# Kernel tuning notes

Hardware: AMD Instinct MI355X
Metric: run time of the kernel (lower is better)

Reference implementation:

```python
import jax, jax.numpy as jnp
import numpy as np

NU = 200000   # num user nodes
NI = 200000   # num item nodes
E = 500000    # edges per relation
D = 128       # in_feats
H = 128       # h_feats
NEG_SLOPE = 0.01  # F.leaky_relu default


def _sage(x_src, x_dst, src, dst, n_dst, W_self, W_neigh, b):
    # DGL SAGEConv('mean'): fc_self(x_dst) + fc_neigh(mean of in-neighbors) + bias
    msg = x_src[src]                                   # [E, d] gather
    agg = jax.ops.segment_sum(msg, dst, num_segments=n_dst)   # [n_dst, d]
    deg = jax.ops.segment_sum(jnp.ones((src.shape[0],), x_src.dtype), dst,
                              num_segments=n_dst)      # [n_dst]
    mean = agg / jnp.maximum(deg, 1.0)[:, None]        # zero in-degree -> 0
    return x_dst @ W_self + mean @ W_neigh + b


def setup_inputs() -> dict:
    key = jax.random.key(0)
    ks = jax.random.split(key, 20)
    s = 1.0 / np.sqrt(D)
    inp = {
        'x_user': jax.random.normal(ks[0], (NU, D), jnp.float32),
        'x_item': jax.random.normal(ks[1], (NI, D), jnp.float32),
        'w1_self_uc': jax.random.normal(ks[2], (D, H), jnp.float32) * s,
        'w1_neigh_uc': jax.random.normal(ks[3], (D, H), jnp.float32) * s,
        'b1_uc': jnp.zeros((H,), jnp.float32),
        'w1_self_iu': jax.random.normal(ks[4], (D, H), jnp.float32) * s,
        'w1_neigh_iu': jax.random.normal(ks[5], (D, H), jnp.float32) * s,
        'b1_iu': jnp.zeros((H,), jnp.float32),
        'w2_self_uc': jax.random.normal(ks[6], (H, H), jnp.float32) * s,
        'w2_neigh_uc': jax.random.normal(ks[7], (H, H), jnp.float32) * s,
        'b2_uc': jnp.zeros((H,), jnp.float32),
        'w2_self_iu': jax.random.normal(ks[8], (H, H), jnp.float32) * s,
        'w2_neigh_iu': jax.random.normal(ks[9], (H, H), jnp.float32) * s,
        'b2_iu': jnp.zeros((H,), jnp.float32),
        'src_uc': jax.random.randint(ks[10], (E,), 0, NU, jnp.int32),
        'dst_uc': jax.random.randint(ks[11], (E,), 0, NI, jnp.int32),
        'src_iu': jax.random.randint(ks[12], (E,), 0, NI, jnp.int32),
        'dst_iu': jax.random.randint(ks[13], (E,), 0, NU, jnp.int32),
    }
    return inp


def reference(x_user, x_item,
              w1_self_uc, w1_neigh_uc, b1_uc, w1_self_iu, w1_neigh_iu, b1_iu,
              w2_self_uc, w2_neigh_uc, b2_uc, w2_self_iu, w2_neigh_iu, b2_iu,
              src_uc, dst_uc, src_iu, dst_iu):
    # layer 1: relation 'clicks' user->item, relation 'clicked_by' item->user
    h1_item = _sage(x_user, x_item, src_uc, dst_uc, NI, w1_self_uc, w1_neigh_uc, b1_uc)
    h1_user = _sage(x_item, x_user, src_iu, dst_iu, NU, w1_self_iu, w1_neigh_iu, b1_iu)
    h1_item = jax.nn.leaky_relu(h1_item, NEG_SLOPE)
    h1_user = jax.nn.leaky_relu(h1_user, NEG_SLOPE)
    # layer 2
    h2_item = _sage(h1_user, h1_item, src_uc, dst_uc, NI, w2_self_uc, w2_neigh_uc, b2_uc)
    h2_user = _sage(h1_item, h1_user, src_iu, dst_iu, NU, w2_self_iu, w2_neigh_iu, b2_iu)
    # stack [user, item] (same shape) for a single output tensor
    return jnp.stack([h2_user, h2_item], axis=0)  # [2, 200000, 128]
```

## Files before the change

kernel.cpp:

```cpp
#include <hip/hip_runtime.h>
#include <hip/hip_bf16.h>

#define D_ 128

typedef __attribute__((ext_vector_type(8))) short s8b;
typedef __attribute__((ext_vector_type(4))) float f4;

union U4 { uint u[4]; s8b v; uint4 q; };

__device__ __forceinline__ void gl16(const void* g, void* lds) {
    __builtin_amdgcn_global_load_lds(
        (const __attribute__((address_space(1))) void*)g,
        (__attribute__((address_space(3))) void*)lds, 16, 0, 0);
}

__device__ __forceinline__ void split2(float f0, float f1, uint& hp, uint& lp) {
    uint u0 = __float_as_uint(f0), u1 = __float_as_uint(f1);
    hp = (u0 >> 16) | (u1 & 0xffff0000u);
    float r0 = f0 - __uint_as_float(u0 & 0xffff0000u);
    float r1 = f1 - __uint_as_float(u1 & 0xffff0000u);
    uint v0 = __float_as_uint(r0), v1 = __float_as_uint(r1);
    uint l0 = (v0 + 0x7fffu + ((v0 >> 16) & 1u)) >> 16;
    uint l1 = (v1 + 0x7fffu + ((v1 >> 16) & 1u)) >> 16;
    lp = l0 | (l1 << 16);
}

__device__ __forceinline__ float4 asf4(uint4 u) {
    return make_float4(__uint_as_float(u.x), __uint_as_float(u.y),
                       __uint_as_float(u.z), __uint_as_float(u.w));
}

__global__ void deg2_kernel(const int* __restrict__ dstA, const int* __restrict__ dstB,
                            int* __restrict__ degA, int* __restrict__ degB, int E) {
    int e = blockIdx.x * blockDim.x + threadIdx.x;
    const int* dst = blockIdx.y ? dstB : dstA;
    int* deg = blockIdx.y ? degB : degA;
    if (e < E) atomicAdd(&deg[dst[e]], 1);
}

__global__ __launch_bounds__(256)
void scan1m(const int* __restrict__ degA, const int* __restrict__ degB,
            int* __restrict__ rpA, int* __restrict__ rpB,
            int* __restrict__ partA, int* __restrict__ partB, int N) {
    const int* deg = blockIdx.y ? degB : degA;
    int* rp = blockIdx.y ? rpB : rpA;
    int* partials = blockIdx.y ? partB : partA;
    int tid = threadIdx.x;
    int i = blockIdx.x * 256 + tid;
    int v = (i < N) ? deg[i] : 0;
    int lane = tid & 63, wid = tid >> 6;
    int x = v;
#pragma unroll
    for (int off = 1; off < 64; off <<= 1) {
        int y = __shfl_up(x, off, 64);
        if (lane >= off) x += y;
    }
    __shared__ int wsum[5];
    if (lane == 63) wsum[wid] = x;
    __syncthreads();
    if (tid == 0) {
        int a = wsum[0], b = wsum[1], c = wsum[2], d = wsum[3];
        wsum[0] = 0; wsum[1] = a; wsum[2] = a + b; wsum[3] = a + b + c;
        wsum[4] = a + b + c + d;
    }
    __syncthreads();
    if (i < N) rp[i] = wsum[wid] + x - v;
    if (tid == 0) partials[blockIdx.x] = wsum[4];
}

__global__ __launch_bounds__(1024)
void scan2m(int* __restrict__ partA, int* __restrict__ partB, int B) {
    int* partials = blockIdx.x ? partB : partA;
    __shared__ int buf[1024];
    int t = threadIdx.x;
    int v = (t < B) ? partials[t] : 0;
    buf[t] = v;
    __syncthreads();
    for (int off = 1; off < 1024; off <<= 1) {
        int add = (t >= off) ? buf[t - off] : 0;
        __syncthreads();
        buf[t] += add;
        __syncthreads();
    }
    if (t < B) partials[t] = buf[t] - v;
}

__global__ __launch_bounds__(256)
void scan3m(int* __restrict__ rpA, int* __restrict__ rpB,
            const int* __restrict__ partA, const int* __restrict__ partB, int N, int E) {
    int* rp = blockIdx.y ? rpB : rpA;
    const int* partials = blockIdx.y ? partB : partA;
    int i = blockIdx.x * 256 + threadIdx.x;
    if (i < N) rp[i] += partials[blockIdx.x];
    if (i == 0) rp[N] = E;
}

__global__ void fill2_csr(const int* __restrict__ srcA, const int* __restrict__ dstA,
                          const int* __restrict__ rpA, int* __restrict__ curA,
                          int* __restrict__ colA, int* __restrict__ colpA,
                          const int* __restrict__ srcB, const int* __restrict__ dstB,
                          const int* __restrict__ rpB, int* __restrict__ curB,
                          int* __restrict__ colB, int* __restrict__ colpB, int E) {
    int e = blockIdx.x * blockDim.x + threadIdx.x;
    if (e >= E) return;
    const int* src = blockIdx.y ? srcB : srcA;
    const int* dst = blockIdx.y ? dstB : dstA;
    const int* rp  = blockIdx.y ? rpB : rpA;
    int* cursor = blockIdx.y ? curB : curA;
    int* col    = blockIdx.y ? colB : colA;
    int* colp   = blockIdx.y ? colpB : colpA;
    int d = dst[e];
    int s = src[e];
    int idx = atomicAdd(&cursor[d], 1);
    col[rp[d] + idx] = s;
    if (idx < 4) colp[d * 4 + idx] = s;
}

__global__ __launch_bounds__(256)
void prep_weights(const float* __restrict__ s0, const float* __restrict__ n0,
                  const float* __restrict__ s1, const float* __restrict__ n1,
                  const float* __restrict__ s2, const float* __restrict__ n2,
                  const float* __restrict__ s3, const float* __restrict__ n3,
                  ushort* __restrict__ WTH, ushort* __restrict__ WTL) {
    int g = blockIdx.y;
    int t = blockIdx.x * 256 + threadIdx.x;
    int c = t & 127;
    int oct = t >> 7;
    const float* self  = g == 0 ? s0 : g == 1 ? s1 : g == 2 ? s2 : s3;
    const float* neigh = g == 0 ? n0 : g == 1 ? n1 : g == 2 ? n2 : n3;
    uint hd[4], ld_[4];
#pragma unroll
    for (int p = 0; p < 4; ++p) {
        uint hpair = 0, lpair = 0;
#pragma unroll
        for (int q = 0; q < 2; ++q) {
            int kv = oct * 8 + p * 2 + q;
            const float* Wsrc = kv < 128 ? self : neigh;
            float f = Wsrc[(size_t)(kv & 127) * 128 + c];
            uint u = __float_as_uint(f);
            uint h = u >> 16;
            float r = f - __uint_as_float(u & 0xffff0000u);
            uint v = __float_as_uint(r);
            uint l = (v + 0x7fffu + ((v >> 16) & 1u)) >> 16;
            hpair |= h << (16 * q);
            lpair |= l << (16 * q);
        }
        hd[p] = hpair; ld_[p] = lpair;
    }
    size_t base = ((size_t)g * 128 + c) * 256 + oct * 8;
    *(uint4*)(WTH + base) = make_uint4(hd[0], hd[1], hd[2], hd[3]);
    *(uint4*)(WTL + base) = make_uint4(ld_[0], ld_[1], ld_[2], ld_[3]);
}

#define AGGH 0
#define AGGL 16384
#define ASTEP 32768
#define WHO 40960
#define WLO 49152

template<int FP32IN, int SPLIT, int LRELU>
__device__ __forceinline__ void fused_body(const char* A1, const char* XN,
        const int* rp, const int* col, const int* colp,
        const ushort* WTh, const ushort* WTl, const float* bias, void* outp,
        int bid, char* smem) {
    const int t = threadIdx.x;
    const int row0 = bid * 64;
    const int li = t & 15;

    uint4 GH[2][4], GL[2][4];
    float wv[2][4];
    int begv[2], endv[2], dgv[2];
#pragma unroll
    for (int p = 0; p < 2; ++p) {
        int nl = p * 32 + (t >> 4);
        int node = row0 + nl;
        int beg = rp[node], end = rp[node + 1];
        int dg = end - beg;
        begv[p] = beg; endv[p] = end; dgv[p] = dg;
        int4 c4 = *(const int4*)(colp + (size_t)node * 4);
        int s0 = dg > 0 ? c4.x : 0;
        int s1 = dg > 1 ? c4.y : 0;
        int s2 = dg > 2 ? c4.z : 0;
        int s3 = dg > 3 ? c4.w : 0;
        wv[p][0] = dg > 0 ? 1.f : 0.f;
        wv[p][1] = dg > 1 ? 1.f : 0.f;
        wv[p][2] = dg > 2 ? 1.f : 0.f;
        wv[p][3] = dg > 3 ? 1.f : 0.f;
        const int lo = FP32IN ? li * 32 : li * 16;
        const int d2 = FP32IN ? 16 : 256;
        const char* p0 = XN + (size_t)s0 * 512 + lo;
        const char* p1 = XN + (size_t)s1 * 512 + lo;
        const char* p2 = XN + (size_t)s2 * 512 + lo;
        const char* p3 = XN + (size_t)s3 * 512 + lo;
        GH[p][0] = *(const uint4*)p0; GL[p][0] = *(const uint4*)(p0 + d2);
        GH[p][1] = *(const uint4*)p1; GL[p][1] = *(const uint4*)(p1 + d2);
        GH[p][2] = *(const uint4*)p2; GL[p][2] = *(const uint4*)(p2 + d2);
        GH[p][3] = *(const uint4*)p3; GL[p][3] = *(const uint4*)(p3 + d2);
    }

    auto stage = [&](int ks) {
        if (ks < 4) {
            if (FP32IN) {
                int row = t >> 3, cs = t & 7;
                gl16(A1 + (size_t)(row0 + row) * 512 + ks * 128 + ((cs ^ (row & 7)) * 16),
                     smem + ASTEP + t * 16);
            } else {
                int j = t & 255, part = t >> 8;
                int row = j >> 2, cs = j & 3;
                gl16(A1 + (size_t)(row0 + row) * 512 + part * 256 + ks * 64
                         + ((cs ^ ((row >> 1) & 3)) * 16),
                     smem + ASTEP + part * 4096 + j * 16);
            }
        }
        {
            int col_ = t >> 2, cs = t & 3;
            size_t so = (size_t)col_ * 512 + ks * 64 + ((cs ^ ((col_ >> 1) & 3)) * 16);
            gl16((const char*)WTh + so, smem + WHO + t * 16);
            gl16((const char*)WTl + so, smem + WLO + t * 16);
        }
    };

    const int w = t >> 6, lane = t & 63;
    const int fr = lane & 15, hi = lane >> 4;
    const int mrow0 = (w & 1) * 32, ncol0 = (w >> 1) * 32;

    f4 acc[2][2];
    {
        float bv[2];
#pragma unroll
        for (int n = 0; n < 2; ++n) bv[n] = bias[ncol0 + n * 16 + fr];
#pragma unroll
        for (int m = 0; m < 2; ++m)
#pragma unroll
            for (int n = 0; n < 2; ++n) acc[m][n] = (f4){bv[n], bv[n], bv[n], bv[n]};
    }

    auto compute = [&](int ks) {
        s8b ah[2], al[2], wh[2], wl[2];
        if (ks < 4) {
            if (FP32IN) {
#pragma unroll
                for (int m = 0; m < 2; ++m) {
                    int r = mrow0 + m * 16 + fr;
                    f4 x0 = *(const f4*)(smem + ASTEP + r * 128 + (((hi * 2) ^ (r & 7)) * 16));
                    f4 x1 = *(const f4*)(smem + ASTEP + r * 128 + (((hi * 2 + 1) ^ (r & 7)) * 16));
                    U4 H, L;
                    split2(x0[0], x0[1], H.u[0], L.u[0]);
                    split2(x0[2], x0[3], H.u[1], L.u[1]);
                    split2(x1[0], x1[1], H.u[2], L.u[2]);
                    split2(x1[2], x1[3], H.u[3], L.u[3]);
                    ah[m] = H.v; al[m] = L.v;
                }
            } else {
#pragma unroll
                for (int m = 0; m < 2; ++m) {
                    int r = mrow0 + m * 16 + fr;
                    int off = r * 64 + ((hi ^ ((r >> 1) & 3)) * 16);
                    ah[m] = *(const s8b*)(smem + ASTEP + off);
                    al[m] = *(const s8b*)(smem + ASTEP + 4096 + off);
                }
            }
        } else {
            int kk = ks - 4;
#pragma unroll
            for (int m = 0; m < 2; ++m) {
                int r = mrow0 + m * 16 + fr;
                int chunk = (kk * 4 + hi) ^ (r & 3) ^ (((r >> 2) & 3) << 2);
                ah[m] = *(const s8b*)(smem + AGGH + r * 256 + chunk * 16);
                al[m] = *(const s8b*)(smem + AGGL + r * 256 + chunk * 16);
            }
        }
#pragma unroll
        for (int n = 0; n < 2; ++n) {
            int c = ncol0 + n * 16 + fr;
            int off = c * 64 + ((hi ^ ((c >> 1) & 3)) * 16);
            wh[n] = *(const s8b*)(smem + WHO + off);
            wl[n] = *(const s8b*)(smem + WLO + off);
        }
#pragma unroll
        for (int n = 0; n < 2; ++n)
#pragma unroll
            for (int m = 0; m < 2; ++m) {
                acc[m][n] = __builtin_amdgcn_mfma_f32_16x16x32_bf16(ah[m], wh[n], acc[m][n], 0, 0, 0);
                acc[m][n] = __builtin_amdgcn_mfma_f32_16x16x32_bf16(al[m], wh[n], acc[m][n], 0, 0, 0);
                acc[m][n] = __builtin_amdgcn_mfma_f32_16x16x32_bf16(ah[m], wl[n], acc[m][n], 0, 0, 0);
            }
    };

    stage(0);
    __syncthreads();

#pragma unroll
    for (int p = 0; p < 2; ++p) {
        int nl = p * 32 + (t >> 4);
        float a[8];
#pragma unroll
        for (int j = 0; j < 8; ++j) a[j] = 0.f;
        if (FP32IN) {
#pragma unroll
            for (int q = 0; q < 4; ++q) {
                float4 X = asf4(GH[p][q]);
                float4 Y = asf4(GL[p][q]);
                float wq = wv[p][q];
                a[0] = fmaf(X.x, wq, a[0]); a[1] = fmaf(X.y, wq, a[1]);
                a[2] = fmaf(X.z, wq, a[2]); a[3] = fmaf(X.w, wq, a[3]);
                a[4] = fmaf(Y.x, wq, a[4]); a[5] = fmaf(Y.y, wq, a[5]);
                a[6] = fmaf(Y.z, wq, a[6]); a[7] = fmaf(Y.w, wq, a[7]);
            }
            for (int e = begv[p] + 4; e < endv[p]; ++e) {
                const char* pp = XN + (size_t)col[e] * 512 + li * 32;
                float4 X = *(const float4*)pp, Y = *(const float4*)(pp + 16);
                a[0] += X.x; a[1] += X.y; a[2] += X.z; a[3] += X.w;
                a[4] += Y.x; a[5] += Y.y; a[6] += Y.z; a[7] += Y.w;
            }
        } else {
#pragma unroll
            for (int q = 0; q < 4; ++q) {
                float wq = wv[p][q];
                const ushort* hu = (const ushort*)&GH[p][q];
                const ushort* lu = (const ushort*)&GL[p][q];
#pragma unroll
                for (int j = 0; j < 8; ++j) {
                    float v = __uint_as_float((uint)hu[j] << 16)
                            + __uint_as_float((uint)lu[j] << 16);
                    a[j] = fmaf(v, wq, a[j]);
                }
            }
            for (int e = begv[p] + 4; e < endv[p]; ++e) {
                const char* pp = XN + (size_t)col[e] * 512 + li * 16;
                uint4 H = *(const uint4*)pp, L = *(const uint4*)(pp + 256);
                const ushort* hu = (const ushort*)&H;
                const ushort* lu = (const ushort*)&L;
#pragma unroll
                for (int j = 0; j < 8; ++j)
                    a[j] += __uint_as_float((uint)hu[j] << 16)
                          + __uint_as_float((uint)lu[j] << 16);
            }
        }
        float inv = 1.f / (float)(dgv[p] > 0 ? dgv[p] : 1);
        uint h[4], l[4];
        split2(a[0] * inv, a[1] * inv, h[0], l[0]);
        split2(a[2] * inv, a[3] * inv, h[1], l[1]);
        split2(a[4] * inv, a[5] * inv, h[2], l[2]);
        split2(a[6] * inv, a[7] * inv, h[3], l[3]);
        int chunk = li ^ (nl & 3) ^ (((nl >> 2) & 3) << 2);
        *(uint4*)(smem + AGGH + nl * 256 + chunk * 16) = make_uint4(h[0], h[1], h[2], h[3]);
        *(uint4*)(smem + AGGL + nl * 256 + chunk * 16) = make_uint4(l[0], l[1], l[2], l[3]);
    }

    compute(0);
    __syncthreads();
    for (int ks = 1; ks < 8; ++ks) {
        stage(ks);
        __syncthreads();
        compute(ks);
        __syncthreads();
    }

    float* T = (float*)smem;
#pragma unroll
    for (int m = 0; m < 2; ++m)
#pragma unroll
        for (int n = 0; n < 2; ++n)
#pragma unroll
            for (int r = 0; r < 4; ++r)
                T[(mrow0 + m * 16 + hi * 4 + r) * 132 + ncol0 + n * 16 + fr] = acc[m][n][r];
    __syncthreads();
    {
        int row = t >> 3, q = t & 7;
        int gr = row0 + row;
        if (SPLIT) {
            char* ob = (char*)outp + (size_t)gr * 512;
#pragma unroll
            for (int i = 0; i < 2; ++i) {
                const float* p = T + row * 132 + (q * 2 + i) * 8;
                f4 x0 = *(const f4*)p;
                f4 x1 = *(const f4*)(p + 4);
                float e[8] = {x0[0], x0[1], x0[2], x0[3], x1[0], x1[1], x1[2], x1[3]};
                if (LRELU) {
#pragma unroll
                    for (int j = 0; j < 8; ++j) e[j] = e[j] > 0.f ? e[j] : 0.01f * e[j];
                }
                uint h[4], l[4];
#pragma unroll
                for (int j = 0; j < 4; ++j) split2(e[2 * j], e[2 * j + 1], h[j], l[j]);
                *(uint4*)(ob + (q * 2 + i) * 16) = make_uint4(h[0], h[1], h[2], h[3]);
                *(uint4*)(ob + 256 + (q * 2 + i) * 16) = make_uint4(l[0], l[1], l[2], l[3]);
            }
        } else {
            float* ob = (float*)outp + (size_t)gr * 128;
#pragma unroll
            for (int i = 0; i < 4; ++i) {
                f4 x = *(const f4*)(T + row * 132 + q * 16 + i * 4);
                float e0 = x[0], e1 = x[1], e2 = x[2], e3 = x[3];
                if (LRELU) {
                    e0 = e0 > 0.f ? e0 : 0.01f * e0;
                    e1 = e1 > 0.f ? e1 : 0.01f * e1;
                    e2 = e2 > 0.f ? e2 : 0.01f * e2;
                    e3 = e3 > 0.f ? e3 : 0.01f * e3;
                }
                *(float4*)(ob + q * 16 + i * 4) = make_float4(e0, e1, e2, e3);
            }
        }
    }
}

template<int FP32IN, int SPLIT, int LRELU>
__global__ __launch_bounds__(512, 4)
void fused2k(const void* A1a, const void* XNa, const int* rpA, const int* colA,
             const int* colpA, const ushort* WTha, const ushort* WTla,
             const float* ba, void* outa,
             const void* A1b, const void* XNb, const int* rpB, const int* colB,
             const int* colpB, const ushort* WThb, const ushort* WTlb,
             const float* bb, void* outb, int blocksA) {
    __shared__ __align__(16) char smem[57344];
    bool isA = (int)blockIdx.x < blocksA;
    int bid = isA ? blockIdx.x : blockIdx.x - blocksA;
    if (isA)
        fused_body<FP32IN, SPLIT, LRELU>((const char*)A1a, (const char*)XNa, rpA, colA,
                                         colpA, WTha, WTla, ba, outa, bid, smem);
    else
        fused_body<FP32IN, SPLIT, LRELU>((const char*)A1b, (const char*)XNb, rpB, colB,
                                         colpB, WThb, WTlb, bb, outb, bid, smem);
}

extern "C" void kernel_launch(void* const* d_in, const int* in_sizes, int n_in,
                              void* d_out, int out_size, void* d_ws, size_t ws_size,
                              hipStream_t stream) {
    const float* x_user     = (const float*)d_in[0];
    const float* x_item     = (const float*)d_in[1];
    const float* w1_self_uc = (const float*)d_in[2];
    const float* w1_neigh_uc= (const float*)d_in[3];
    const float* b1_uc      = (const float*)d_in[4];
    const float* w1_self_iu = (const float*)d_in[5];
    const float* w1_neigh_iu= (const float*)d_in[6];
    const float* b1_iu      = (const float*)d_in[7];
    const float* w2_self_uc = (const float*)d_in[8];
    const float* w2_neigh_uc= (const float*)d_in[9];
    const float* b2_uc      = (const float*)d_in[10];
    const float* w2_self_iu = (const float*)d_in[11];
    const float* w2_neigh_iu= (const float*)d_in[12];
    const float* b2_iu      = (const float*)d_in[13];
    const int* src_uc = (const int*)d_in[14];
    const int* dst_uc = (const int*)d_in[15];
    const int* src_iu = (const int*)d_in[16];
    const int* dst_iu = (const int*)d_in[17];

    const int NU = in_sizes[0] / D_;
    const int NI = in_sizes[1] / D_;
    const int E  = in_sizes[14];

    float* f_user = (float*)d_out;
    float* f_item = (float*)d_out + (size_t)NU * 128;

    char* ws = (char*)d_ws;
    const size_t FEAT_BYTES = (size_t)200000 * 512;
    char* h1_item  = ws;          ws += FEAT_BYTES;
    char* h1_user  = ws;          ws += FEAT_BYTES;
    ushort* WTH    = (ushort*)ws; ws += (size_t)4 * 128 * 256 * sizeof(ushort);
    ushort* WTL    = (ushort*)ws; ws += (size_t)4 * 128 * 256 * sizeof(ushort);
    int* colp_uc   = (int*)ws;    ws += (size_t)200000 * 4 * sizeof(int);
    int* colp_iu   = (int*)ws;    ws += (size_t)200000 * 4 * sizeof(int);
    int* rp_uc     = (int*)ws;    ws += (size_t)(NI + 1) * sizeof(int);
    int* rp_iu     = (int*)ws;    ws += (size_t)(NU + 1) * sizeof(int);
    int* col_uc    = (int*)ws;    ws += (size_t)E * sizeof(int);
    int* col_iu    = (int*)ws;    ws += (size_t)E * sizeof(int);
    int* deg_uc    = (int*)ws;    ws += (size_t)200000 * sizeof(int);
    int* deg_iu    = (int*)ws;    ws += (size_t)200000 * sizeof(int);
    int* cur_uc    = (int*)ws;    ws += (size_t)200000 * sizeof(int);
    int* cur_iu    = (int*)ws;    ws += (size_t)200000 * sizeof(int);
    int* partA     = (int*)ws;    ws += (size_t)1024 * sizeof(int);
    int* partB     = (int*)ws;    ws += (size_t)1024 * sizeof(int);

    const int TPB = 256;
    const int eBlocks  = (E + TPB - 1) / TPB;
    const int sBlocks  = (200000 + 255) / 256;
    const int mBlocksI = (NI + 63) / 64;
    const int mBlocksU = (NU + 63) / 64;
    const size_t WSTRIDE = (size_t)128 * 256;

    hipMemsetAsync(deg_uc, 0, (size_t)4 * 200000 * sizeof(int), stream);

    prep_weights<<<dim3(16, 4), 256, 0, stream>>>(
        w1_self_uc, w1_neigh_uc, w1_self_iu, w1_neigh_iu,
        w2_self_uc, w2_neigh_uc, w2_self_iu, w2_neigh_iu, WTH, WTL);

    deg2_kernel<<<dim3(eBlocks, 2), TPB, 0, stream>>>(dst_uc, dst_iu, deg_uc, deg_iu, E);
    scan1m<<<dim3(sBlocks, 2), 256, 0, stream>>>(deg_uc, deg_iu, rp_uc, rp_iu, partA, partB, 200000);
    scan2m<<<2, 1024, 0, stream>>>(partA, partB, sBlocks);
    scan3m<<<dim3(sBlocks, 2), 256, 0, stream>>>(rp_uc, rp_iu, partA, partB, 200000, E);
    fill2_csr<<<dim3(eBlocks, 2), TPB, 0, stream>>>(src_uc, dst_uc, rp_uc, cur_uc, col_uc, colp_uc,
                                                    src_iu, dst_iu, rp_iu, cur_iu, col_iu, colp_iu, E);

    fused2k<1, 1, 1><<<mBlocksI + mBlocksU, 512, 0, stream>>>(
        x_item, x_user, rp_uc, col_uc, colp_uc, WTH + 0 * WSTRIDE, WTL + 0 * WSTRIDE,
        b1_uc, h1_item,
        x_user, x_item, rp_iu, col_iu, colp_iu, WTH + 1 * WSTRIDE, WTL + 1 * WSTRIDE,
        b1_iu, h1_user, mBlocksI);

    fused2k<0, 0, 0><<<mBlocksI + mBlocksU, 512, 0, stream>>>(
        h1_item, h1_user, rp_uc, col_uc, colp_uc, WTH + 2 * WSTRIDE, WTL + 2 * WSTRIDE,
        b2_uc, f_item,
        h1_user, h1_item, rp_iu, col_iu, colp_iu, WTH + 3 * WSTRIDE, WTL + 3 * WSTRIDE,
        b2_iu, f_user, mBlocksI);
}
```

Measured before the change: 582.9 us.

## Halve fused SAGE block tile to 32 rows with 256 threads

Each fused aggregation+GEMM block now covers 32 destination rows with 256 threads (4 waves, each owning 32 output columns) instead of 64 rows with 512 threads, and LDS usage drops from 56KB to 36KB. The neighbor mean is now fully computed and written to LDS before the k-loop starts, instead of holding prefetched gathers in registers while the first weight/activation stage is in flight. The smaller tile is meant to raise occupancy and cut per-thread register pressure. In exchange, weight tiles are staged twice as often per output row, and the gather latency no longer overlaps with the first stage load.

```diff
diff --git a/kernel.cpp b/kernel.cpp
--- a/kernel.cpp
+++ b/kernel.cpp
@@ -153,10 +153,10 @@
 }
 
 #define AGGH 0
-#define AGGL 16384
-#define ASTEP 32768
-#define WHO 40960
-#define WLO 49152
+#define AGGL 8192
+#define ASTEP 16384
+#define WHO 20480
+#define WLO 28672
 
 template<int FP32IN, int SPLIT, int LRELU>
 __device__ __forceinline__ void fused_body(const char* A1, const char* XN,
@@ -164,38 +164,105 @@
         const ushort* WTh, const ushort* WTl, const float* bias, void* outp,
         int bid, char* smem) {
     const int t = threadIdx.x;
-    const int row0 = bid * 64;
+    const int row0 = bid * 32;
     const int li = t & 15;
 
-    uint4 GH[2][4], GL[2][4];
-    float wv[2][4];
-    int begv[2], endv[2], dgv[2];
 #pragma unroll
     for (int p = 0; p < 2; ++p) {
-        int nl = p * 32 + (t >> 4);
+        int nl = p * 16 + (t >> 4);
         int node = row0 + nl;
         int beg = rp[node], end = rp[node + 1];
         int dg = end - beg;
-        begv[p] = beg; endv[p] = end; dgv[p] = dg;
         int4 c4 = *(const int4*)(colp + (size_t)node * 4);
         int s0 = dg > 0 ? c4.x : 0;
         int s1 = dg > 1 ? c4.y : 0;
         int s2 = dg > 2 ? c4.z : 0;
         int s3 = dg > 3 ? c4.w : 0;
-        wv[p][0] = dg > 0 ? 1.f : 0.f;
-        wv[p][1] = dg > 1 ? 1.f : 0.f;
-        wv[p][2] = dg > 2 ? 1.f : 0.f;
-        wv[p][3] = dg > 3 ? 1.f : 0.f;
+        float w0 = dg > 0 ? 1.f : 0.f;
+        float w1 = dg > 1 ? 1.f : 0.f;
+        float w2 = dg > 2 ? 1.f : 0.f;
+        float w3 = dg > 3 ? 1.f : 0.f;
+        float a[8];
+#pragma unroll
+        for (int j = 0; j < 8; ++j) a[j] = 0.f;
         const int lo = FP32IN ? li * 32 : li * 16;
         const int d2 = FP32IN ? 16 : 256;
         const char* p0 = XN + (size_t)s0 * 512 + lo;
         const char* p1 = XN + (size_t)s1 * 512 + lo;
         const char* p2 = XN + (size_t)s2 * 512 + lo;
         const char* p3 = XN + (size_t)s3 * 512 + lo;
-        GH[p][0] = *(const uint4*)p0; GL[p][0] = *(const uint4*)(p0 + d2);
-        GH[p][1] = *(const uint4*)p1; GL[p][1] = *(const uint4*)(p1 + d2);
-        GH[p][2] = *(const uint4*)p2; GL[p][2] = *(const uint4*)(p2 + d2);
-        GH[p][3] = *(const uint4*)p3; GL[p][3] = *(const uint4*)(p3 + d2);
+        uint4 H0 = *(const uint4*)p0, L0 = *(const uint4*)(p0 + d2);
+        uint4 H1 = *(const uint4*)p1, L1 = *(const uint4*)(p1 + d2);
+        uint4 H2 = *(const uint4*)p2, L2 = *(const uint4*)(p2 + d2);
+        uint4 H3 = *(const uint4*)p3, L3 = *(const uint4*)(p3 + d2);
+        if (FP32IN) {
+#pragma unroll
+            for (int q = 0; q < 4; ++q) {
+                uint4 Hq = q == 0 ? H0 : q == 1 ? H1 : q == 2 ? H2 : H3;
+                uint4 Lq = q == 0 ? L0 : q == 1 ? L1 : q == 2 ? L2 : L3;
+                float wq = q == 0 ? w0 : q == 1 ? w1 : q == 2 ? w2 : w3;
+                float4 X = asf4(Hq), Y = asf4(Lq);
+                a[0] = fmaf(X.x, wq, a[0]); a[1] = fmaf(X.y, wq, a[1]);
+                a[2] = fmaf(X.z, wq, a[2]); a[3] = fmaf(X.w, wq, a[3]);
+                a[4] = fmaf(Y.x, wq, a[4]); a[5] = fmaf(Y.y, wq, a[5]);
+                a[6] = fmaf(Y.z, wq, a[6]); a[7] = fmaf(Y.w, wq, a[7]);
+            }
+            for (int e = beg + 4; e < end; ++e) {
+                const char* pp = XN + (size_t)col[e] * 512 + li * 32;
+                float4 X = *(const float4*)pp, Y = *(const float4*)(pp + 16);
+                a[0] += X.x; a[1] += X.y; a[2] += X.z; a[3] += X.w;
+                a[4] += Y.x; a[5] += Y.y; a[6] += Y.z; a[7] += Y.w;
+            }
+        } else {
+#pragma unroll
+            for (int q = 0; q < 4; ++q) {
+                uint4 Hq = q == 0 ? H0 : q == 1 ? H1 : q == 2 ? H2 : H3;
+                uint4 Lq = q == 0 ? L0 : q == 1 ? L1 : q == 2 ? L2 : L3;
+                float wq = q == 0 ? w0 : q == 1 ? w1 : q == 2 ? w2 : w3;
+                const ushort* hu = (const ushort*)&Hq;
+                const ushort* lu = (const ushort*)&Lq;
+#pragma unroll
+                for (int j = 0; j < 8; ++j) {
+                    float v = __uint_as_float((uint)hu[j] << 16)
+                            + __uint_as_float((uint)lu[j] << 16);
+                    a[j] = fmaf(v, wq, a[j]);
+                }
+            }
+            for (int e = beg + 4; e < end; ++e) {
+                const char* pp = XN + (size_t)col[e] * 512 + li * 16;
+                uint4 H = *(const uint4*)pp, L = *(const uint4*)(pp + 256);
+                const ushort* hu = (const ushort*)&H;
+                const ushort* lu = (const ushort*)&L;
+#pragma unroll
+                for (int j = 0; j < 8; ++j)
+                    a[j] += __uint_as_float((uint)hu[j] << 16)
+                          + __uint_as_float((uint)lu[j] << 16);
+            }
+        }
+        float inv = 1.f / (float)(dg > 0 ? dg : 1);
+        uint h[4], l[4];
+        split2(a[0] * inv, a[1] * inv, h[0], l[0]);
+        split2(a[2] * inv, a[3] * inv, h[1], l[1]);
+        split2(a[4] * inv, a[5] * inv, h[2], l[2]);
+        split2(a[6] * inv, a[7] * inv, h[3], l[3]);
+        int chunk = li ^ (nl & 3) ^ (((nl >> 2) & 3) << 2);
+        *(uint4*)(smem + AGGH + nl * 256 + chunk * 16) = make_uint4(h[0], h[1], h[2], h[3]);
+        *(uint4*)(smem + AGGL + nl * 256 + chunk * 16) = make_uint4(l[0], l[1], l[2], l[3]);
+    }
+
+    const int w = t >> 6, lane = t & 63;
+    const int fr = lane & 15, hi = lane >> 4;
+    const int ncol0 = w * 32;
+
+    f4 acc[2][2];
+    {
+        float bv[2];
+#pragma unroll
+        for (int n = 0; n < 2; ++n) bv[n] = bias[ncol0 + n * 16 + fr];
+#pragma unroll
+        for (int m = 0; m < 2; ++m)
+#pragma unroll
+            for (int n = 0; n < 2; ++n) acc[m][n] = (f4){bv[n], bv[n], bv[n], bv[n]};
     }
 
     auto stage = [&](int ks) {
@@ -205,35 +272,22 @@
                 gl16(A1 + (size_t)(row0 + row) * 512 + ks * 128 + ((cs ^ (row & 7)) * 16),
                      smem + ASTEP + t * 16);
             } else {
-                int j = t & 255, part = t >> 8;
+                int j = t & 127, part = t >> 7;
                 int row = j >> 2, cs = j & 3;
                 gl16(A1 + (size_t)(row0 + row) * 512 + part * 256 + ks * 64
                          + ((cs ^ ((row >> 1) & 3)) * 16),
-                     smem + ASTEP + part * 4096 + j * 16);
-            }
-        }
-        {
-            int col_ = t >> 2, cs = t & 3;
+                     smem + ASTEP + part * 2048 + j * 16);
+            }
+        }
+#pragma unroll
+        for (int it = 0; it < 2; ++it) {
+            int j = it * 256 + t;
+            int col_ = j >> 2, cs = j & 3;
             size_t so = (size_t)col_ * 512 + ks * 64 + ((cs ^ ((col_ >> 1) & 3)) * 16);
-            gl16((const char*)WTh + so, smem + WHO + t * 16);
-            gl16((const char*)WTl + so, smem + WLO + t * 16);
+            gl16((const char*)WTh + so, smem + WHO + j * 16);
+            gl16((const char*)WTl + so, smem + WLO + j * 16);
         }
     };
-
-    const int w = t >> 6, lane = t & 63;
-    const int fr = lane & 15, hi = lane >> 4;
-    const int mrow0 = (w & 1) * 32, ncol0 = (w >> 1) * 32;
-
-    f4 acc[2][2];
-    {
-        float bv[2];
-#pragma unroll
-        for (int n = 0; n < 2; ++n) bv[n] = bias[ncol0 + n * 16 + fr];
-#pragma unroll
-        for (int m = 0; m < 2; ++m)
-#pragma unroll
-            for (int n = 0; n < 2; ++n) acc[m][n] = (f4){bv[n], bv[n], bv[n], bv[n]};
-    }
 
     auto compute = [&](int ks) {
         s8b ah[2], al[2], wh[2], wl[2];
@@ -241,7 +295,7 @@
             if (FP32IN) {
 #pragma unroll
                 for (int m = 0; m < 2; ++m) {
-                    int r = mrow0 + m * 16 + fr;
+                    int r = m * 16 + fr;
                     f4 x0 = *(const f4*)(smem + ASTEP + r * 128 + (((hi * 2) ^ (r & 7)) * 16));
                     f4 x1 = *(const f4*)(smem + ASTEP + r * 128 + (((hi * 2 + 1) ^ (r & 7)) * 16));
                     U4 H, L;
@@ -254,17 +308,17 @@
             } else {
 #pragma unroll
                 for (int m = 0; m < 2; ++m) {
-                    int r = mrow0 + m * 16 + fr;
+                    int r = m * 16 + fr;
                     int off = r * 64 + ((hi ^ ((r >> 1) & 3)) * 16);
                     ah[m] = *(const s8b*)(smem + ASTEP + off);
-                    al[m] = *(const s8b*)(smem + ASTEP + 4096 + off);
+                    al[m] = *(const s8b*)(smem + ASTEP + 2048 + off);
                 }
             }
         } else {
             int kk = ks - 4;
 #pragma unroll
             for (int m = 0; m < 2; ++m) {
-                int r = mrow0 + m * 16 + fr;
+                int r = m * 16 + fr;
                 int chunk = (kk * 4 + hi) ^ (r & 3) ^ (((r >> 2) & 3) << 2);
                 ah[m] = *(const s8b*)(smem + AGGH + r * 256 + chunk * 16);
                 al[m] = *(const s8b*)(smem + AGGL + r * 256 + chunk * 16);
@@ -287,70 +341,7 @@
             }
     };
 
-    stage(0);
-    __syncthreads();
-
-#pragma unroll
-    for (int p = 0; p < 2; ++p) {
-        int nl = p * 32 + (t >> 4);
-        float a[8];
-#pragma unroll
-        for (int j = 0; j < 8; ++j) a[j] = 0.f;
-        if (FP32IN) {
-#pragma unroll
-            for (int q = 0; q < 4; ++q) {
-                float4 X = asf4(GH[p][q]);
-                float4 Y = asf4(GL[p][q]);
-                float wq = wv[p][q];
-                a[0] = fmaf(X.x, wq, a[0]); a[1] = fmaf(X.y, wq, a[1]);
-                a[2] = fmaf(X.z, wq, a[2]); a[3] = fmaf(X.w, wq, a[3]);
-                a[4] = fmaf(Y.x, wq, a[4]); a[5] = fmaf(Y.y, wq, a[5]);
-                a[6] = fmaf(Y.z, wq, a[6]); a[7] = fmaf(Y.w, wq, a[7]);
-            }
-            for (int e = begv[p] + 4; e < endv[p]; ++e) {
-                const char* pp = XN + (size_t)col[e] * 512 + li * 32;
-                float4 X = *(const float4*)pp, Y = *(const float4*)(pp + 16);
-                a[0] += X.x; a[1] += X.y; a[2] += X.z; a[3] += X.w;
-                a[4] += Y.x; a[5] += Y.y; a[6] += Y.z; a[7] += Y.w;
-            }
-        } else {
-#pragma unroll
-            for (int q = 0; q < 4; ++q) {
-                float wq = wv[p][q];
-                const ushort* hu = (const ushort*)&GH[p][q];
-                const ushort* lu = (const ushort*)&GL[p][q];
-#pragma unroll
-                for (int j = 0; j < 8; ++j) {
-                    float v = __uint_as_float((uint)hu[j] << 16)
-                            + __uint_as_float((uint)lu[j] << 16);
-                    a[j] = fmaf(v, wq, a[j]);
-                }
-            }
-            for (int e = begv[p] + 4; e < endv[p]; ++e) {
-                const char* pp = XN + (size_t)col[e] * 512 + li * 16;
-                uint4 H = *(const uint4*)pp, L = *(const uint4*)(pp + 256);
-                const ushort* hu = (const ushort*)&H;
-                const ushort* lu = (const ushort*)&L;
-#pragma unroll
-                for (int j = 0; j < 8; ++j)
-                    a[j] += __uint_as_float((uint)hu[j] << 16)
-                          + __uint_as_float((uint)lu[j] << 16);
-            }
-        }
-        float inv = 1.f / (float)(dgv[p] > 0 ? dgv[p] : 1);
-        uint h[4], l[4];
-        split2(a[0] * inv, a[1] * inv, h[0], l[0]);
-        split2(a[2] * inv, a[3] * inv, h[1], l[1]);
-        split2(a[4] * inv, a[5] * inv, h[2], l[2]);
-        split2(a[6] * inv, a[7] * inv, h[3], l[3]);
-        int chunk = li ^ (nl & 3) ^ (((nl >> 2) & 3) << 2);
-        *(uint4*)(smem + AGGH + nl * 256 + chunk * 16) = make_uint4(h[0], h[1], h[2], h[3]);
-        *(uint4*)(smem + AGGL + nl * 256 + chunk * 16) = make_uint4(l[0], l[1], l[2], l[3]);
-    }
-
-    compute(0);
-    __syncthreads();
-    for (int ks = 1; ks < 8; ++ks) {
+    for (int ks = 0; ks < 8; ++ks) {
         stage(ks);
         __syncthreads();
         compute(ks);
@@ -364,7 +355,7 @@
         for (int n = 0; n < 2; ++n)
 #pragma unroll
             for (int r = 0; r < 4; ++r)
-                T[(mrow0 + m * 16 + hi * 4 + r) * 132 + ncol0 + n * 16 + fr] = acc[m][n][r];
+                T[(m * 16 + hi * 4 + r) * 132 + ncol0 + n * 16 + fr] = acc[m][n][r];
     __syncthreads();
     {
         int row = t >> 3, q = t & 7;
@@ -406,14 +397,14 @@
 }
 
 template<int FP32IN, int SPLIT, int LRELU>
-__global__ __launch_bounds__(512, 4)
+__global__ __launch_bounds__(256, 4)
 void fused2k(const void* A1a, const void* XNa, const int* rpA, const int* colA,
              const int* colpA, const ushort* WTha, const ushort* WTla,
              const float* ba, void* outa,
              const void* A1b, const void* XNb, const int* rpB, const int* colB,
              const int* colpB, const ushort* WThb, const ushort* WTlb,
              const float* bb, void* outb, int blocksA) {
-    __shared__ __align__(16) char smem[57344];
+    __shared__ __align__(16) char smem[36864];
     bool isA = (int)blockIdx.x < blocksA;
     int bid = isA ? blockIdx.x : blockIdx.x - blocksA;
     if (isA)
@@ -475,8 +466,8 @@
     const int TPB = 256;
     const int eBlocks  = (E + TPB - 1) / TPB;
     const int sBlocks  = (200000 + 255) / 256;
-    const int mBlocksI = (NI + 63) / 64;
-    const int mBlocksU = (NU + 63) / 64;
+    const int mBlocksI = (NI + 31) / 32;
+    const int mBlocksU = (NU + 31) / 32;
     const size_t WSTRIDE = (size_t)128 * 256;
 
     hipMemsetAsync(deg_uc, 0, (size_t)4 * 200000 * sizeof(int), stream);
@@ -492,13 +483,13 @@
     fill2_csr<<<dim3(eBlocks, 2), TPB, 0, stream>>>(src_uc, dst_uc, rp_uc, cur_uc, col_uc, colp_uc,
                                                     src_iu, dst_iu, rp_iu, cur_iu, col_iu, colp_iu, E);
 
-    fused2k<1, 1, 1><<<mBlocksI + mBlocksU, 512, 0, stream>>>(
+    fused2k<1, 1, 1><<<mBlocksI + mBlocksU, 256, 0, stream>>>(
         x_item, x_user, rp_uc, col_uc, colp_uc, WTH + 0 * WSTRIDE, WTL + 0 * WSTRIDE,
         b1_uc, h1_item,
         x_user, x_item, rp_iu, col_iu, colp_iu, WTH + 1 * WSTRIDE, WTL + 1 * WSTRIDE,
         b1_iu, h1_user, mBlocksI);
 
-    fused2k<0, 0, 0><<<mBlocksI + mBlocksU, 512, 0, stream>>>(
+    fused2k<0, 0, 0><<<mBlocksI + mBlocksU, 256, 0, stream>>>(
         h1_item, h1_user, rp_uc, col_uc, colp_uc, WTH + 2 * WSTRIDE, WTL + 2 * WSTRIDE,
         b2_uc, f_item,
         h1_user, h1_item, rp_iu, col_iu, colp_iu, WTH + 3 * WSTRIDE, WTL + 3 * WSTRIDE,
```

Result: slower. 628.8 us (+7.9%).
